# Optimization experiments

Hardware: AMD Instinct MI355X
Metric: run time of the kernel (lower is better)

## Reference

```python
import jax, jax.numpy as jnp
import numpy as np
from jax import lax

# module constants (match init_kwargs)
CHUNK_LENGTH = 32
RIGHT_CONTEXT_LENGTH = 8
CHANNELS = 512
KERNEL_SIZE = 31
CACHE_SIZE = KERNEL_SIZE - 1  # 30


def _conv1d(x, w, b, groups=1):
    # x: (N, C_in, L), w: (C_out, C_in/groups, K), b: (C_out,)
    y = lax.conv_general_dilated(
        x, w, window_strides=(1,), padding='VALID',
        dimension_numbers=('NCH', 'OIH', 'NCH'),
        feature_group_count=groups)
    return y + b[None, :, None]


def setup_inputs() -> dict:
    key = jax.random.key(0)
    ks = jax.random.split(key, 9)
    U, B, D, R = 2048, 16, CHANNELS, 512
    s = 0.02
    return {
        'utterance': jax.random.normal(ks[0], (U, B, D), jnp.float32),
        'right_context': jax.random.normal(ks[1], (R, B, D), jnp.float32),
        'cache': jnp.zeros((B, D, CACHE_SIZE), jnp.float32),
        'w1': jax.random.normal(ks[2], (2 * D, D, 1), jnp.float32) * s,
        'b1': jax.random.normal(ks[3], (2 * D,), jnp.float32) * s,
        'wd': jax.random.normal(ks[4], (D, 1, KERNEL_SIZE), jnp.float32) * s,
        'bd': jax.random.normal(ks[5], (D,), jnp.float32) * s,
        'w2': jax.random.normal(ks[6], (D, D, 1), jnp.float32) * s,
        'b2': jax.random.normal(ks[7], (D,), jnp.float32) * s,
    }


def reference(utterance, right_context, cache, w1, b1, wd, bd, w2, b2):
    U, B, D = utterance.shape
    R = right_context.shape[0]
    rcl, cl, cs = RIGHT_CONTEXT_LENGTH, CHUNK_LENGTH, CACHE_SIZE

    # concat [right_context; utterance] along time, to (B, D, R+U)
    x = jnp.concatenate([right_context, utterance], axis=0).transpose(1, 2, 0)
    # pointwise_conv1 (ScaledConv1d == plain conv in forward math) + GLU
    # (ActivationBalancer is identity in forward)
    x = _conv1d(x, w1, b1)  # (B, 2D, R+U)
    a, g = jnp.split(x, 2, axis=1)
    x = a * jax.nn.sigmoid(g)  # GLU -> (B, D, R+U)

    utt = x[:, :, R:]      # (B, D, U)
    rc = x[:, :, :R]       # (B, D, R)

    # causal depthwise conv with left cache
    pad_utt = jnp.concatenate([cache, utt], axis=2)  # (B, D, cs+U)
    new_cache = pad_utt[:, :, -cs:]
    utt = _conv1d(pad_utt, wd, bd, groups=D)  # (B, D, U)

    # _split_right_context: gather per-chunk left cache for each rc segment
    U_ = cs + U
    num_chunks = R // rcl
    pad_utt_t = pad_utt.transpose(2, 0, 1)   # (U_, B, D)
    rc_t = rc.transpose(2, 0, 1)             # (R, B, D)
    end_idx = jnp.minimum(U_, cs + (jnp.arange(num_chunks) + 1) * cl)
    start_idx = end_idx - cs                 # (num_chunks,)
    gidx = start_idx[:, None] + jnp.arange(cs)[None, :]   # (nc, cs)
    padding = pad_utt_t[gidx]                # (nc, cs, B, D)
    padding = padding.transpose(0, 2, 1, 3).reshape(num_chunks * B, cs, D)
    rc_seg = rc_t.reshape(num_chunks, rcl, B, D).transpose(0, 2, 1, 3)
    rc_seg = rc_seg.reshape(num_chunks * B, rcl, D)
    pad_rc = jnp.concatenate([padding, rc_seg], axis=1).transpose(0, 2, 1)  # (nc*B, D, cs+rcl)
    rc_out = _conv1d(pad_rc, wd, bd, groups=D)  # (nc*B, D, rcl)
    # _merge_right_context
    rc_out = rc_out.reshape(num_chunks, B, D, rcl).transpose(1, 2, 0, 3)
    rc_out = rc_out.reshape(B, D, R)

    x = jnp.concatenate([rc_out, utt], axis=2)  # (B, D, R+U)
    # DoubleSwish: x * sigmoid(x - 1)
    x = x * jax.nn.sigmoid(x - 1.0)
    x = _conv1d(x, w2, b2)  # pointwise_conv2

    rc_final = x[:, :, :R].transpose(2, 0, 1)   # (R, B, D)
    utt_final = x[:, :, R:].transpose(2, 0, 1)  # (U, B, D)
    return utt_final, rc_final, new_cache
```

## Files before the change

### kernel.cpp

```cpp
#include <hip/hip_runtime.h>
#include <math.h>

#define B_SZ 16
#define D_CH 512
#define U_LEN 2048
#define R_LEN 512
#define T_LEN 2560
#define KS 31
#define CS 30

typedef __attribute__((ext_vector_type(8))) short short8;
typedef __attribute__((ext_vector_type(4))) float floatx4;

__device__ __forceinline__ float bf2f(ushort u) {
    unsigned v = (unsigned)u << 16;
    float f; __builtin_memcpy(&f, &v, 4); return f;
}
__device__ __forceinline__ ushort f2bf(float f) {
    unsigned v; __builtin_memcpy(&v, &f, 4);
    v += 0x7fff + ((v >> 16) & 1);
    return (ushort)(v >> 16);
}
__device__ __forceinline__ float sigmoidf_(float x) { return 1.0f / (1.0f + __expf(-x)); }

__device__ __forceinline__ void gld16(const void* g, void* l) {
    __builtin_amdgcn_global_load_lds((const __attribute__((address_space(1))) void*)g,
                                     (__attribute__((address_space(3))) void*)l, 16, 0, 0);
}

__global__ __launch_bounds__(256) void k_conv_all(
    const float* __restrict__ utt, const float* __restrict__ rc, const float* __restrict__ cache,
    const float* __restrict__ w1, const float* __restrict__ w2, const float* __restrict__ wd,
    ushort* __restrict__ xb, ushort* __restrict__ w1b, ushort* __restrict__ w2b,
    ushort* __restrict__ pu, float* __restrict__ wdT)
{
    int blk = blockIdx.x;
    if (blk < 5120) {
        size_t f4 = (size_t)blk * 1024 + threadIdx.x * 4;
        size_t o = f4 * 4;
        int q = (int)(o >> 9), d = (int)(o & 511);
        const float* src = (q < 8192) ? rc + ((size_t)q << 9) + d
                                      : utt + (((size_t)(q - 8192)) << 9) + d;
        ushort* dst = xb + o;
        #pragma unroll
        for (int i = 0; i < 4; ++i) {
            float4 v = ((const float4*)src)[i];
            ushort4 u4; u4.x = f2bf(v.x); u4.y = f2bf(v.y); u4.z = f2bf(v.z); u4.w = f2bf(v.w);
            ((ushort4*)dst)[i] = u4;
        }
    } else if (blk < 5312) {
        int t = (blk - 5120) * 1024 + threadIdx.x * 4;
        if (t < 131072) {
            #pragma unroll
            for (int i = 0; i < 4; ++i) {
                int e = (t + i) << 2;
                int row = e >> 9, k = e & 511;
                int rr = row & 511;
                int rp = (rr >> 4) * 32 + ((row >> 9) << 4) + (rr & 15);
                float4 v = ((const float4*)w1)[t + i];
                ushort4 u4; u4.x = f2bf(v.x); u4.y = f2bf(v.y); u4.z = f2bf(v.z); u4.w = f2bf(v.w);
                ((ushort4*)w1b)[rp * 128 + (k >> 2)] = u4;
            }
        } else {
            int t2 = t - 131072;
            #pragma unroll
            for (int i = 0; i < 4; ++i) {
                float4 v = ((const float4*)w2)[t2 + i];
                ushort4 u4; u4.x = f2bf(v.x); u4.y = f2bf(v.y); u4.z = f2bf(v.z); u4.w = f2bf(v.w);
                ((ushort4*)w2b)[t2 + i] = u4;
            }
        }
    } else if (blk < 6272) {
        int o = (blk - 5312) * 256 + threadIdx.x;
        int d = o & 511, p = o >> 13, b = (o >> 9) & 15;
        pu[o] = f2bf(cache[((size_t)b * D_CH + d) * CS + p]);
    } else {
        int idx = (blk - 6272) * 256 + threadIdx.x;
        int k = idx >> 9, d = idx & 511;
        wdT[idx] = wd[(size_t)d * KS + k];
    }
}

__global__ __launch_bounds__(256, 2) void k1_mfma(
    const ushort* __restrict__ xb, const ushort* __restrict__ w1p,
    const float* __restrict__ b1, ushort* __restrict__ yr, ushort* __restrict__ pu)
{
    __shared__ __attribute__((aligned(16))) ushort lds[4][2][4096];
    const int tid = threadIdx.x;
    const int w = tid >> 6, lane = tid & 63;
    const int col = lane & 15, quad = lane >> 4;
    const int wm = w >> 1, wn = w & 1;
    const int bid = blockIdx.x;
    const int f = (bid & 7) * 320 + (bid >> 3);
    const int mt = f >> 3, nn = f & 7;
    const int q0 = mt * 128, n0 = nn * 128;

    floatx4 acc[4][4];
    #pragma unroll
    for (int i = 0; i < 4; ++i)
        #pragma unroll
        for (int j = 0; j < 4; ++j) acc[i][j] = 0.f;

    int offA[4], offB[4];
    #pragma unroll
    for (int i = 0; i < 4; ++i) {
        int rA = wm * 64 + i * 16 + col;
        offA[i] = rA * 64 + ((quad ^ ((rA >> 1) & 3)) << 4);
        int rB = wn * 64 + i * 16 + col;
        offB[i] = rB * 64 + ((quad ^ ((rB >> 1) & 3)) << 4);
    }

    const int srow = tid >> 2;
    const int sqs = (tid & 3) ^ ((srow >> 1) & 3);
    const ushort* gA0 = xb  + (((size_t)(q0 + srow))      << 9) + (sqs << 3);
    const ushort* gA1 = xb  + (((size_t)(q0 + 64 + srow)) << 9) + (sqs << 3);
    const ushort* gB0 = w1p + (((size_t)(n0 + srow))      << 9) + (sqs << 3);
    const ushort* gB1 = w1p + (((size_t)(n0 + 64 + srow)) << 9) + (sqs << 3);

#define STAGE1(t_, bi_) do { \
        const int kc_ = (t_) << 5; \
        gld16(gA0 + kc_, &lds[bi_][0][w * 512]); \
        gld16(gA1 + kc_, &lds[bi_][0][2048 + w * 512]); \
        gld16(gB0 + kc_, &lds[bi_][1][w * 512]); \
        gld16(gB1 + kc_, &lds[bi_][1][2048 + w * 512]); \
    } while (0)

    STAGE1(0, 0); STAGE1(1, 1); STAGE1(2, 2);

    #pragma unroll
    for (int s = 0; s < 16; ++s) {
        if (s < 14)       asm volatile("s_waitcnt vmcnt(8)\n\ts_barrier" ::: "memory");
        else if (s == 14) asm volatile("s_waitcnt vmcnt(4)\n\ts_barrier" ::: "memory");
        else              asm volatile("s_waitcnt vmcnt(0)\n\ts_barrier" ::: "memory");
        if (s < 13) STAGE1(s + 3, (s + 3) & 3);
        const char* A  = (const char*)&lds[s & 3][0][0];
        const char* Bp = (const char*)&lds[s & 3][1][0];
        short8 af[4], bf8[4];
        #pragma unroll
        for (int i = 0; i < 4; ++i) af[i]  = *(const short8*)(A + offA[i]);
        #pragma unroll
        for (int j = 0; j < 4; ++j) bf8[j] = *(const short8*)(Bp + offB[j]);
        __builtin_amdgcn_s_setprio(1);
        #pragma unroll
        for (int i = 0; i < 4; ++i)
            #pragma unroll
            for (int j = 0; j < 4; ++j)
                acc[i][j] = __builtin_amdgcn_mfma_f32_16x16x32_bf16(af[i], bf8[j], acc[i][j], 0, 0, 0);
        __builtin_amdgcn_s_setprio(0);
    }
#undef STAGE1

    ushort* dst = (q0 < 8192) ? yr : pu;
    const int qb = (q0 < 8192) ? q0 : (q0 - 7712);
    const int nb2 = (n0 + wn * 64) >> 1;
    #pragma unroll
    for (int fe = 0; fe < 2; ++fe) {
        const int na = nb2 + fe * 16 + col;
        const float ba = b1[na], bg = b1[512 + na];
        #pragma unroll
        for (int i = 0; i < 4; ++i) {
            const int row = qb + wm * 64 + i * 16 + quad * 4;
            #pragma unroll
            for (int r = 0; r < 4; ++r) {
                float a = acc[i][2 * fe][r] + ba;
                float g = acc[i][2 * fe + 1][r] + bg;
                dst[(((size_t)(row + r)) << 9) + na] = f2bf(a * sigmoidf_(g));
            }
        }
    }
}

__global__ __launch_bounds__(256) void k2_fused(
    const ushort* __restrict__ pu, const ushort* __restrict__ yr,
    const float* __restrict__ wdT, const float* __restrict__ bd,
    ushort* __restrict__ z, float* __restrict__ out)
{
    const int tid = threadIdx.x;
    const int bid = blockIdx.x;
    if (bid < 8192) {
        const int ug = bid & 255, b = (bid >> 8) & 15, dh = bid >> 12;
        const int d = dh * 256 + tid;
        const int u0 = ug * 8;
        float wreg[31];
        #pragma unroll
        for (int k = 0; k < 31; ++k) wreg[k] = wdT[k * 512 + d];
        const float bias = bd[d];
        float acc[8];
        #pragma unroll
        for (int i = 0; i < 8; ++i) acc[i] = bias;
        const ushort* base = pu + (((size_t)u0 * 16 + b) << 9) + d;
        #pragma unroll
        for (int p = 0; p < 38; ++p) {
            float v = bf2f(base[(size_t)p * 8192]);
            #pragma unroll
            for (int i = 0; i < 8; ++i) {
                int k = p - i;
                if (k >= 0 && k < 31) acc[i] = fmaf(wreg[k], v, acc[i]);
            }
        }
        ushort* zp = z + d;
        #pragma unroll
        for (int i = 0; i < 8; ++i) {
            float v = acc[i];
            v = v * sigmoidf_(v - 1.0f);
            zp[((size_t)((R_LEN + u0 + i) * 16 + b)) << 9] = f2bf(v);
        }
        if (ug == 255) {
            float* outc = out + 20971520 + ((size_t)b * 512 + d) * 30;
            #pragma unroll
            for (int p = 8; p < 38; ++p)
                outc[p - 8] = bf2f(base[(size_t)p * 8192]);
        }
    } else {
        const int m = bid - 8192;
        const int ci = m & 63, b = (m >> 6) & 15, dh = m >> 10;
        const int d = dh * 256 + tid;
        float wreg[31];
        #pragma unroll
        for (int k = 0; k < 31; ++k) wreg[k] = wdT[k * 512 + d];
        const float bias = bd[d];
        float acc[8];
        #pragma unroll
        for (int j = 0; j < 8; ++j) acc[j] = bias;
        #pragma unroll
        for (int r = 0; r < 38; ++r) {
            const ushort* src = (r < 30)
                ? pu + (((size_t)((32 * ci + 32 + r) * 16 + b)) << 9) + d
                : yr + (((size_t)(((8 * ci) + (r - 30)) * 16 + b)) << 9) + d;
            float v = bf2f(*src);
            #pragma unroll
            for (int j = 0; j < 8; ++j) {
                int k = r - j;
                if (k >= 0 && k < 31) acc[j] = fmaf(wreg[k], v, acc[j]);
            }
        }
        #pragma unroll
        for (int j = 0; j < 8; ++j) {
            float v = acc[j];
            v = v * sigmoidf_(v - 1.0f);
            z[(((size_t)((ci * 8 + j) * 16 + b)) << 9) + d] = f2bf(v);
        }
    }
}

__global__ __launch_bounds__(256, 2) void k3_mfma(
    const ushort* __restrict__ zb, const ushort* __restrict__ w2b,
    const float* __restrict__ b2, float* __restrict__ out)
{
    __shared__ __attribute__((aligned(16))) ushort lds[4][2][4096];
    const int tid = threadIdx.x;
    const int w = tid >> 6, lane = tid & 63;
    const int col = lane & 15, quad = lane >> 4;
    const int wm = w >> 1, wn = w & 1;
    const int bid = blockIdx.x;
    const int f = (bid & 7) * 160 + (bid >> 3);
    const int mt = f >> 2, nn = f & 3;
    const int q0 = mt * 128, n0 = nn * 128;

    floatx4 acc[4][4];
    #pragma unroll
    for (int i = 0; i < 4; ++i)
        #pragma unroll
        for (int j = 0; j < 4; ++j) acc[i][j] = 0.f;

    int offA[4], offB[4];
    #pragma unroll
    for (int i = 0; i < 4; ++i) {
        int rA = wm * 64 + i * 16 + col;
        offA[i] = rA * 64 + ((quad ^ ((rA >> 1) & 3)) << 4);
        int rB = wn * 64 + i * 16 + col;
        offB[i] = rB * 64 + ((quad ^ ((rB >> 1) & 3)) << 4);
    }

    const int srow = tid >> 2;
    const int sqs = (tid & 3) ^ ((srow >> 1) & 3);
    const ushort* gA0 = zb  + (((size_t)(q0 + srow))      << 9) + (sqs << 3);
    const ushort* gA1 = zb  + (((size_t)(q0 + 64 + srow)) << 9) + (sqs << 3);
    const ushort* gB0 = w2b + (((size_t)(n0 + srow))      << 9) + (sqs << 3);
    const ushort* gB1 = w2b + (((size_t)(n0 + 64 + srow)) << 9) + (sqs << 3);

#define STAGE3(t_, bi_) do { \
        const int kc_ = (t_) << 5; \
        gld16(gA0 + kc_, &lds[bi_][0][w * 512]); \
        gld16(gA1 + kc_, &lds[bi_][0][2048 + w * 512]); \
        gld16(gB0 + kc_, &lds[bi_][1][w * 512]); \
        gld16(gB1 + kc_, &lds[bi_][1][2048 + w * 512]); \
    } while (0)

    STAGE3(0, 0); STAGE3(1, 1); STAGE3(2, 2);

    #pragma unroll
    for (int s = 0; s < 16; ++s) {
        if (s < 14)       asm volatile("s_waitcnt vmcnt(8)\n\ts_barrier" ::: "memory");
        else if (s == 14) asm volatile("s_waitcnt vmcnt(4)\n\ts_barrier" ::: "memory");
        else              asm volatile("s_waitcnt vmcnt(0)\n\ts_barrier" ::: "memory");
        if (s < 13) STAGE3(s + 3, (s + 3) & 3);
        const char* A  = (const char*)&lds[s & 3][0][0];
        const char* Bp = (const char*)&lds[s & 3][1][0];
        short8 af[4], bf8[4];
        #pragma unroll
        for (int i = 0; i < 4; ++i) af[i]  = *(const short8*)(A + offA[i]);
        #pragma unroll
        for (int j = 0; j < 4; ++j) bf8[j] = *(const short8*)(Bp + offB[j]);
        __builtin_amdgcn_s_setprio(1);
        #pragma unroll
        for (int i = 0; i < 4; ++i)
            #pragma unroll
            for (int j = 0; j < 4; ++j)
                acc[i][j] = __builtin_amdgcn_mfma_f32_16x16x32_bf16(af[i], bf8[j], acc[i][j], 0, 0, 0);
        __builtin_amdgcn_s_setprio(0);
    }
#undef STAGE3

    #pragma unroll
    for (int j = 0; j < 4; ++j) {
        const int n = n0 + wn * 64 + j * 16 + col;
        const float bb = b2[n];
        #pragma unroll
        for (int i = 0; i < 4; ++i) {
            const int qrow = q0 + wm * 64 + i * 16 + quad * 4;
            #pragma unroll
            for (int r = 0; r < 4; ++r) {
                const int q = qrow + r;
                float v = acc[i][j][r] + bb;
                size_t off = (q < 8192) ? (size_t)16777216 + ((size_t)q << 9)
                                        : ((size_t)(q - 8192) << 9);
                out[off + n] = v;
            }
        }
    }
}

extern "C" void kernel_launch(void* const* d_in, const int* in_sizes, int n_in,
                              void* d_out, int out_size, void* d_ws, size_t ws_size,
                              hipStream_t stream)
{
    const float* utt   = (const float*)d_in[0];
    const float* rc    = (const float*)d_in[1];
    const float* cache = (const float*)d_in[2];
    const float* w1    = (const float*)d_in[3];
    const float* b1    = (const float*)d_in[4];
    const float* wd    = (const float*)d_in[5];
    const float* bd    = (const float*)d_in[6];
    const float* w2    = (const float*)d_in[7];
    const float* b2    = (const float*)d_in[8];
    float* out = (float*)d_out;

    ushort* xb  = (ushort*)d_ws;
    ushort* zb  = xb  + (size_t)20971520;
    ushort* pu  = zb  + (size_t)20971520;
    ushort* yr  = pu  + (size_t)17039360;
    ushort* w1b = yr  + (size_t)4194304;
    ushort* w2b = w1b + (size_t)524288;
    float*  wdT = (float*)(w2b + (size_t)262144);

    k_conv_all<<<dim3(6334), 256, 0, stream>>>(utt, rc, cache, w1, w2, wd, xb, w1b, w2b, pu, wdT);
    k1_mfma   <<<dim3(2560), 256, 0, stream>>>(xb, w1b, b1, yr, pu);
    k2_fused  <<<dim3(10240), 256, 0, stream>>>(pu, yr, wdT, bd, zb, out);
    k3_mfma   <<<dim3(1280), 256, 0, stream>>>(zb, w2b, b2, out);
}
```

Before: 294.8 us.

## Enlarge first pointwise GEMM tile to 256x256 with 8 waves and split-phase pipeline

```diff
diff --git a/kernel.cpp b/kernel.cpp
--- a/kernel.cpp
+++ b/kernel.cpp
@@ -27,6 +27,9 @@
     __builtin_amdgcn_global_load_lds((const __attribute__((address_space(1))) void*)g,
                                      (__attribute__((address_space(3))) void*)l, 16, 0, 0);
 }
+
+#define BAR()    asm volatile("s_barrier" ::: "memory")
+#define LGKM0()  do { asm volatile("s_waitcnt lgkmcnt(0)" ::: "memory"); __builtin_amdgcn_sched_barrier(0); } while (0)
 
 __global__ __launch_bounds__(256) void k_conv_all(
     const float* __restrict__ utt, const float* __restrict__ rc, const float* __restrict__ cache,
@@ -81,74 +84,124 @@
     }
 }
 
-__global__ __launch_bounds__(256, 2) void k1_mfma(
+__global__ __launch_bounds__(512, 1) void k1_mfma(
     const ushort* __restrict__ xb, const ushort* __restrict__ w1p,
     const float* __restrict__ b1, ushort* __restrict__ yr, ushort* __restrict__ pu)
 {
-    __shared__ __attribute__((aligned(16))) ushort lds[4][2][4096];
+    __shared__ __attribute__((aligned(16))) ushort lds[2][4][8192];
     const int tid = threadIdx.x;
     const int w = tid >> 6, lane = tid & 63;
     const int col = lane & 15, quad = lane >> 4;
-    const int wm = w >> 1, wn = w & 1;
+    const int wm = w >> 2, wn = w & 3;
     const int bid = blockIdx.x;
-    const int f = (bid & 7) * 320 + (bid >> 3);
-    const int mt = f >> 3, nn = f & 7;
-    const int q0 = mt * 128, n0 = nn * 128;
-
-    floatx4 acc[4][4];
-    #pragma unroll
-    for (int i = 0; i < 4; ++i)
+    const int f = (bid & 7) * 80 + (bid >> 3);
+    const int mt = f >> 2, nt = f & 3;
+    const int q0 = mt * 256, n0 = nt * 256;
+
+    floatx4 acc[8][4];
+    #pragma unroll
+    for (int i = 0; i < 8; ++i)
         #pragma unroll
         for (int j = 0; j < 4; ++j) acc[i][j] = 0.f;
 
-    int offA[4], offB[4];
-    #pragma unroll
-    for (int i = 0; i < 4; ++i) {
-        int rA = wm * 64 + i * 16 + col;
-        offA[i] = rA * 64 + ((quad ^ ((rA >> 1) & 3)) << 4);
-        int rB = wn * 64 + i * 16 + col;
-        offB[i] = rB * 64 + ((quad ^ ((rB >> 1) & 3)) << 4);
-    }
-
-    const int srow = tid >> 2;
-    const int sqs = (tid & 3) ^ ((srow >> 1) & 3);
-    const ushort* gA0 = xb  + (((size_t)(q0 + srow))      << 9) + (sqs << 3);
-    const ushort* gA1 = xb  + (((size_t)(q0 + 64 + srow)) << 9) + (sqs << 3);
-    const ushort* gB0 = w1p + (((size_t)(n0 + srow))      << 9) + (sqs << 3);
-    const ushort* gB1 = w1p + (((size_t)(n0 + 64 + srow)) << 9) + (sqs << 3);
-
-#define STAGE1(t_, bi_) do { \
-        const int kc_ = (t_) << 5; \
-        gld16(gA0 + kc_, &lds[bi_][0][w * 512]); \
-        gld16(gA1 + kc_, &lds[bi_][0][2048 + w * 512]); \
-        gld16(gB0 + kc_, &lds[bi_][1][w * 512]); \
-        gld16(gB1 + kc_, &lds[bi_][1][2048 + w * 512]); \
+    int offA[8], offB[4];
+    #pragma unroll
+    for (int i = 0; i < 8; ++i) {
+        int r = wm * 128 + i * 16 + col;
+        offA[i] = r * 64 + ((quad ^ ((r >> 1) & 3)) << 4);
+    }
+    #pragma unroll
+    for (int j = 0; j < 4; ++j) {
+        int r = wn * 64 + j * 16 + col;
+        offB[j] = r * 64 + ((quad ^ ((r >> 1) & 3)) << 4);
+    }
+
+    const int rA = w * 32 + (lane >> 2);
+    const int cA = (lane & 3) ^ ((rA >> 1) & 3);
+    const ushort* gA0 = xb  + (((size_t)(q0 + rA)) << 9) + cA * 8;
+    const ushort* gA1 = gA0 + (16 << 9);
+    const ushort* gB0 = w1p + (((size_t)(n0 + rA)) << 9) + cA * 8;
+    const ushort* gB1 = gB0 + (16 << 9);
+    const int sl0 = (w * 2) * 512, sl1 = (w * 2 + 1) * 512;
+
+#define STG(bk_, h_, p0_, p1_, ko_) do { \
+        gld16((p0_) + (ko_), &lds[bk_][h_][sl0]); \
+        gld16((p1_) + (ko_), &lds[bk_][h_][sl1]); \
     } while (0)
 
-    STAGE1(0, 0); STAGE1(1, 1); STAGE1(2, 2);
-
-    #pragma unroll
-    for (int s = 0; s < 16; ++s) {
-        if (s < 14)       asm volatile("s_waitcnt vmcnt(8)\n\ts_barrier" ::: "memory");
-        else if (s == 14) asm volatile("s_waitcnt vmcnt(4)\n\ts_barrier" ::: "memory");
-        else              asm volatile("s_waitcnt vmcnt(0)\n\ts_barrier" ::: "memory");
-        if (s < 13) STAGE1(s + 3, (s + 3) & 3);
-        const char* A  = (const char*)&lds[s & 3][0][0];
-        const char* Bp = (const char*)&lds[s & 3][1][0];
-        short8 af[4], bf8[4];
-        #pragma unroll
-        for (int i = 0; i < 4; ++i) af[i]  = *(const short8*)(A + offA[i]);
-        #pragma unroll
-        for (int j = 0; j < 4; ++j) bf8[j] = *(const short8*)(Bp + offB[j]);
-        __builtin_amdgcn_s_setprio(1);
-        #pragma unroll
-        for (int i = 0; i < 4; ++i)
-            #pragma unroll
-            for (int j = 0; j < 4; ++j)
-                acc[i][j] = __builtin_amdgcn_mfma_f32_16x16x32_bf16(af[i], bf8[j], acc[i][j], 0, 0, 0);
-        __builtin_amdgcn_s_setprio(0);
-    }
-#undef STAGE1
+    STG(0, 0, gA0, gA1, 0); STG(0, 1, gB0, gB1, 0);
+    STG(0, 2, gA0, gA1, 32); STG(0, 3, gB0, gB1, 32);
+    asm volatile("s_waitcnt vmcnt(4)" ::: "memory");
+    BAR();
+
+    #pragma unroll 2
+    for (int t = 0; t < 8; ++t) {
+        const int tb = t & 1, nb = tb ^ 1;
+        const int st = (t < 7);
+        const int kc = (t + 1) << 6;
+        const char* A0 = (const char*)&lds[tb][0][0];
+        const char* B0 = (const char*)&lds[tb][1][0];
+        const char* A1 = (const char*)&lds[tb][2][0];
+        const char* B1 = (const char*)&lds[tb][3][0];
+        {
+            short8 a[8], b[4];
+            #pragma unroll
+            for (int i = 0; i < 8; ++i) a[i] = *(const short8*)(A0 + offA[i]);
+            #pragma unroll
+            for (int j = 0; j < 4; ++j) b[j] = *(const short8*)(B0 + offB[j]);
+            if (st) STG(nb, 0, gA0, gA1, kc);
+            BAR(); LGKM0();
+            __builtin_amdgcn_s_setprio(1);
+            #pragma unroll
+            for (int i = 0; i < 8; ++i) {
+                acc[i][0] = __builtin_amdgcn_mfma_f32_16x16x32_bf16(a[i], b[0], acc[i][0], 0, 0, 0);
+                acc[i][1] = __builtin_amdgcn_mfma_f32_16x16x32_bf16(a[i], b[1], acc[i][1], 0, 0, 0);
+            }
+            __builtin_amdgcn_s_setprio(0);
+            BAR();
+            if (st) STG(nb, 1, gB0, gB1, kc);
+            BAR();
+            __builtin_amdgcn_s_setprio(1);
+            #pragma unroll
+            for (int i = 0; i < 8; ++i) {
+                acc[i][2] = __builtin_amdgcn_mfma_f32_16x16x32_bf16(a[i], b[2], acc[i][2], 0, 0, 0);
+                acc[i][3] = __builtin_amdgcn_mfma_f32_16x16x32_bf16(a[i], b[3], acc[i][3], 0, 0, 0);
+            }
+            __builtin_amdgcn_s_setprio(0);
+            if (st) asm volatile("s_waitcnt vmcnt(4)" ::: "memory");
+            else    asm volatile("s_waitcnt vmcnt(0)" ::: "memory");
+            BAR();
+        }
+        {
+            short8 a[8], b[4];
+            #pragma unroll
+            for (int i = 0; i < 8; ++i) a[i] = *(const short8*)(A1 + offA[i]);
+            #pragma unroll
+            for (int j = 0; j < 4; ++j) b[j] = *(const short8*)(B1 + offB[j]);
+            if (st) STG(nb, 2, gA0, gA1, kc + 32);
+            BAR(); LGKM0();
+            __builtin_amdgcn_s_setprio(1);
+            #pragma unroll
+            for (int i = 0; i < 8; ++i) {
+                acc[i][0] = __builtin_amdgcn_mfma_f32_16x16x32_bf16(a[i], b[0], acc[i][0], 0, 0, 0);
+                acc[i][1] = __builtin_amdgcn_mfma_f32_16x16x32_bf16(a[i], b[1], acc[i][1], 0, 0, 0);
+            }
+            __builtin_amdgcn_s_setprio(0);
+            BAR();
+            if (st) STG(nb, 3, gB0, gB1, kc + 32);
+            BAR();
+            __builtin_amdgcn_s_setprio(1);
+            #pragma unroll
+            for (int i = 0; i < 8; ++i) {
+                acc[i][2] = __builtin_amdgcn_mfma_f32_16x16x32_bf16(a[i], b[2], acc[i][2], 0, 0, 0);
+                acc[i][3] = __builtin_amdgcn_mfma_f32_16x16x32_bf16(a[i], b[3], acc[i][3], 0, 0, 0);
+            }
+            __builtin_amdgcn_s_setprio(0);
+            if (st) asm volatile("s_waitcnt vmcnt(4)" ::: "memory");
+            BAR();
+        }
+    }
+#undef STG
 
     ushort* dst = (q0 < 8192) ? yr : pu;
     const int qb = (q0 < 8192) ? q0 : (q0 - 7712);
@@ -158,8 +211,8 @@
         const int na = nb2 + fe * 16 + col;
         const float ba = b1[na], bg = b1[512 + na];
         #pragma unroll
-        for (int i = 0; i < 4; ++i) {
-            const int row = qb + wm * 64 + i * 16 + quad * 4;
+        for (int i = 0; i < 8; ++i) {
+            const int row = qb + wm * 128 + i * 16 + quad * 4;
             #pragma unroll
             for (int r = 0; r < 4; ++r) {
                 float a = acc[i][2 * fe][r] + ba;
@@ -355,7 +408,7 @@
     float*  wdT = (float*)(w2b + (size_t)262144);
 
     k_conv_all<<<dim3(6334), 256, 0, stream>>>(utt, rc, cache, w1, w2, wd, xb, w1b, w2b, pu, wdT);
-    k1_mfma   <<<dim3(2560), 256, 0, stream>>>(xb, w1b, b1, yr, pu);
+    k1_mfma   <<<dim3(640), 512, 0, stream>>>(xb, w1b, b1, yr, pu);
     k2_fused  <<<dim3(10240), 256, 0, stream>>>(pu, yr, wdT, bd, zb, out);
     k3_mfma   <<<dim3(1280), 256, 0, stream>>>(zb, w2b, b2, out);
 }
```

Result: slower. 314.7 us (+6.7%).

## Make k1 GEMM persistent over five tiles with cross-tile prefetch

Applied to the files above, without the earlier changes.

```diff
diff --git a/kernel.cpp b/kernel.cpp
--- a/kernel.cpp
+++ b/kernel.cpp
@@ -91,9 +91,7 @@
     const int col = lane & 15, quad = lane >> 4;
     const int wm = w >> 1, wn = w & 1;
     const int bid = blockIdx.x;
-    const int f = (bid & 7) * 320 + (bid >> 3);
-    const int mt = f >> 3, nn = f & 7;
-    const int q0 = mt * 128, n0 = nn * 128;
+    const int fbase = (bid & 7) * 320 + (bid >> 3) * 5;
 
     floatx4 acc[4][4];
     #pragma unroll
@@ -112,62 +110,91 @@
 
     const int srow = tid >> 2;
     const int sqs = (tid & 3) ^ ((srow >> 1) & 3);
-    const ushort* gA0 = xb  + (((size_t)(q0 + srow))      << 9) + (sqs << 3);
-    const ushort* gA1 = xb  + (((size_t)(q0 + 64 + srow)) << 9) + (sqs << 3);
-    const ushort* gB0 = w1p + (((size_t)(n0 + srow))      << 9) + (sqs << 3);
-    const ushort* gB1 = w1p + (((size_t)(n0 + 64 + srow)) << 9) + (sqs << 3);
-
-#define STAGE1(t_, bi_) do { \
-        const int kc_ = (t_) << 5; \
-        gld16(gA0 + kc_, &lds[bi_][0][w * 512]); \
-        gld16(gA1 + kc_, &lds[bi_][0][2048 + w * 512]); \
-        gld16(gB0 + kc_, &lds[bi_][1][w * 512]); \
-        gld16(gB1 + kc_, &lds[bi_][1][2048 + w * 512]); \
+
+    int q0 = (fbase >> 3) * 128, n0 = (fbase & 7) * 128;
+    const ushort* gA0 = xb  + (((size_t)(q0 + srow)) << 9) + (sqs << 3);
+    const ushort* gA1 = gA0 + ((size_t)64 << 9);
+    const ushort* gB0 = w1p + (((size_t)(n0 + srow)) << 9) + (sqs << 3);
+    const ushort* gB1 = gB0 + ((size_t)64 << 9);
+
+#define STAGE1(pA0_, pA1_, pB0_, pB1_, st_) do { \
+        const int kc_ = (st_) << 5; \
+        const int bi_ = (st_) & 3; \
+        gld16((pA0_) + kc_, &lds[bi_][0][w * 512]); \
+        gld16((pA1_) + kc_, &lds[bi_][0][2048 + w * 512]); \
+        gld16((pB0_) + kc_, &lds[bi_][1][w * 512]); \
+        gld16((pB1_) + kc_, &lds[bi_][1][2048 + w * 512]); \
     } while (0)
-
-    STAGE1(0, 0); STAGE1(1, 1); STAGE1(2, 2);
-
-    #pragma unroll
-    for (int s = 0; s < 16; ++s) {
-        if (s < 14)       asm volatile("s_waitcnt vmcnt(8)\n\ts_barrier" ::: "memory");
-        else if (s == 14) asm volatile("s_waitcnt vmcnt(4)\n\ts_barrier" ::: "memory");
-        else              asm volatile("s_waitcnt vmcnt(0)\n\ts_barrier" ::: "memory");
-        if (s < 13) STAGE1(s + 3, (s + 3) & 3);
-        const char* A  = (const char*)&lds[s & 3][0][0];
-        const char* Bp = (const char*)&lds[s & 3][1][0];
-        short8 af[4], bf8[4];
-        #pragma unroll
-        for (int i = 0; i < 4; ++i) af[i]  = *(const short8*)(A + offA[i]);
-        #pragma unroll
-        for (int j = 0; j < 4; ++j) bf8[j] = *(const short8*)(Bp + offB[j]);
-        __builtin_amdgcn_s_setprio(1);
+#define WB(n_) asm volatile("s_waitcnt vmcnt(" #n_ ")\n\ts_barrier" ::: "memory")
+
+    STAGE1(gA0, gA1, gB0, gB1, 0);
+    STAGE1(gA0, gA1, gB0, gB1, 1);
+    STAGE1(gA0, gA1, gB0, gB1, 2);
+
+    #pragma unroll 1
+    for (int t = 0; t < 5; ++t) {
+        const int f1 = (t < 4) ? (fbase + t + 1) : fbase;
+        const int q0n = (f1 >> 3) * 128, n0n = (f1 & 7) * 128;
+        const ushort* nA0 = xb  + (((size_t)(q0n + srow)) << 9) + (sqs << 3);
+        const ushort* nA1 = nA0 + ((size_t)64 << 9);
+        const ushort* nB0 = w1p + (((size_t)(n0n + srow)) << 9) + (sqs << 3);
+        const ushort* nB1 = nB0 + ((size_t)64 << 9);
+
+        #pragma unroll
+        for (int s = 0; s < 16; ++s) {
+            if (s < 3)        { if (t) WB(44); else WB(8); }
+            else if (s < 14)  { WB(8); }
+            else if (s == 14) { if (t < 4) WB(8); else WB(4); }
+            else              { if (t < 4) WB(8); else WB(0); }
+
+            if (s < 13)     STAGE1(gA0, gA1, gB0, gB1, s + 3);
+            else if (t < 4) STAGE1(nA0, nA1, nB0, nB1, s - 13);
+
+            const char* A  = (const char*)&lds[s & 3][0][0];
+            const char* Bp = (const char*)&lds[s & 3][1][0];
+            short8 af[4], bf8[4];
+            #pragma unroll
+            for (int i = 0; i < 4; ++i) af[i]  = *(const short8*)(A + offA[i]);
+            #pragma unroll
+            for (int j = 0; j < 4; ++j) bf8[j] = *(const short8*)(Bp + offB[j]);
+            __builtin_amdgcn_s_setprio(1);
+            #pragma unroll
+            for (int i = 0; i < 4; ++i)
+                #pragma unroll
+                for (int j = 0; j < 4; ++j)
+                    acc[i][j] = __builtin_amdgcn_mfma_f32_16x16x32_bf16(af[i], bf8[j], acc[i][j], 0, 0, 0);
+            __builtin_amdgcn_s_setprio(0);
+        }
+
+        {
+            ushort* dst = (q0 < 8192) ? yr : pu;
+            const int qb = (q0 < 8192) ? q0 : (q0 - 7712);
+            const int nb2 = (n0 + wn * 64) >> 1;
+            #pragma unroll
+            for (int fe = 0; fe < 2; ++fe) {
+                const int na = nb2 + fe * 16 + col;
+                const float ba = b1[na], bg = b1[512 + na];
+                #pragma unroll
+                for (int i = 0; i < 4; ++i) {
+                    const int row = qb + wm * 64 + i * 16 + quad * 4;
+                    #pragma unroll
+                    for (int r = 0; r < 4; ++r) {
+                        float a = acc[i][2 * fe][r] + ba;
+                        float g = acc[i][2 * fe + 1][r] + bg;
+                        dst[(((size_t)(row + r)) << 9) + na] = f2bf(a * sigmoidf_(g));
+                    }
+                }
+            }
+        }
+        q0 = q0n; n0 = n0n;
+        gA0 = nA0; gA1 = nA1; gB0 = nB0; gB1 = nB1;
         #pragma unroll
         for (int i = 0; i < 4; ++i)
             #pragma unroll
-            for (int j = 0; j < 4; ++j)
-                acc[i][j] = __builtin_amdgcn_mfma_f32_16x16x32_bf16(af[i], bf8[j], acc[i][j], 0, 0, 0);
-        __builtin_amdgcn_s_setprio(0);
+            for (int j = 0; j < 4; ++j) acc[i][j] = 0.f;
     }
 #undef STAGE1
-
-    ushort* dst = (q0 < 8192) ? yr : pu;
-    const int qb = (q0 < 8192) ? q0 : (q0 - 7712);
-    const int nb2 = (n0 + wn * 64) >> 1;
-    #pragma unroll
-    for (int fe = 0; fe < 2; ++fe) {
-        const int na = nb2 + fe * 16 + col;
-        const float ba = b1[na], bg = b1[512 + na];
-        #pragma unroll
-        for (int i = 0; i < 4; ++i) {
-            const int row = qb + wm * 64 + i * 16 + quad * 4;
-            #pragma unroll
-            for (int r = 0; r < 4; ++r) {
-                float a = acc[i][2 * fe][r] + ba;
-                float g = acc[i][2 * fe + 1][r] + bg;
-                dst[(((size_t)(row + r)) << 9) + na] = f2bf(a * sigmoidf_(g));
-            }
-        }
-    }
+#undef WB
 }
 
 __global__ __launch_bounds__(256) void k2_fused(
@@ -355,7 +382,7 @@
     float*  wdT = (float*)(w2b + (size_t)262144);
 
     k_conv_all<<<dim3(6334), 256, 0, stream>>>(utt, rc, cache, w1, w2, wd, xb, w1b, w2b, pu, wdT);
-    k1_mfma   <<<dim3(2560), 256, 0, stream>>>(xb, w1b, b1, yr, pu);
+    k1_mfma   <<<dim3(512), 256, 0, stream>>>(xb, w1b, b1, yr, pu);
     k2_fused  <<<dim3(10240), 256, 0, stream>>>(pu, yr, wdT, bd, zb, out);
     k3_mfma   <<<dim3(1280), 256, 0, stream>>>(zb, w2b, b2, out);
 }
```

Result: no change. 297.6 us (+1.0%).
